# Optimization experiments

Hardware: AMD Instinct MI355X
Metric: run time of the kernel (lower is better)

## Reference

```python
import jax, jax.numpy as jnp
import numpy as np

TAU = 2.0        # LIFNode tau
ALPHA = 4.0      # spikingjelly default surrogate Sigmoid alpha
EPS = 1e-5       # BatchNorm eps
NUM_HEADS = 8

@jax.custom_vjp
def spike(u):
    # Heaviside with sigmoid surrogate gradient (spikingjelly default)
    return (u >= 0.0).astype(u.dtype)

def _spike_fwd(u):
    return spike(u), u

def _spike_bwd(u, g):
    s = jax.nn.sigmoid(ALPHA * u)
    return (g * ALPHA * s * (1.0 - s),)

spike.defvjp(_spike_fwd, _spike_bwd)

def lif(x, vth=1.0):
    # single-step LIF from rest (v=0, v_reset=0, decay_input=True): v = x / tau
    return spike(x / TAU - vth)

def conv1x1_bn(x, w, gamma, beta, mean, var):
    # 1x1 conv (no bias) + eval-mode BatchNorm, fused affine
    y = jnp.einsum('oc,bchw->bohw', w, x)
    inv = gamma / jnp.sqrt(var + EPS)
    return y * inv[None, :, None, None] + (beta - mean * inv)[None, :, None, None]


def setup_inputs() -> dict:
    B, C, H, W = 16, 768, 32, 32
    key = jax.random.key(0)
    ks = jax.random.split(key, 22)
    def bn(i):
        return (jax.random.uniform(ks[i], (C,)) + 0.5,
                0.1 * jax.random.normal(ks[i + 1], (C,)),
                0.1 * jax.random.normal(ks[i + 2], (C,)),
                jax.random.uniform(ks[i + 3], (C,)) + 0.5)
    q_gamma, q_beta, q_mean, q_var = bn(1)
    k_gamma, k_beta, k_mean, k_var = bn(5)
    v_gamma, v_beta, v_mean, v_var = bn(9)
    p_gamma, p_beta, p_mean, p_var = bn(13)
    W_SCALE = 0.25  # keeps post-BN activations spanning the LIF threshold
    return {
        'x': 3.0 * jax.random.normal(ks[0], (B, C, H, W), dtype=jnp.float32),
        'wq': W_SCALE * jax.random.normal(ks[17], (C, C), dtype=jnp.float32),
        'q_gamma': q_gamma, 'q_beta': q_beta, 'q_mean': q_mean, 'q_var': q_var,
        'wk': W_SCALE * jax.random.normal(ks[18], (C, C), dtype=jnp.float32),
        'k_gamma': k_gamma, 'k_beta': k_beta, 'k_mean': k_mean, 'k_var': k_var,
        'wv': W_SCALE * jax.random.normal(ks[19], (C, C), dtype=jnp.float32),
        'v_gamma': v_gamma, 'v_beta': v_beta, 'v_mean': v_mean, 'v_var': v_var,
        'wp': W_SCALE * jax.random.normal(ks[20], (C, C), dtype=jnp.float32),
        'bp': 0.1 * jax.random.normal(ks[21], (C,), dtype=jnp.float32),
        'p_gamma': p_gamma, 'p_beta': p_beta, 'p_mean': p_mean, 'p_var': p_var,
    }


def reference(x, wq, q_gamma, q_beta, q_mean, q_var,
              wk, k_gamma, k_beta, k_mean, k_var,
              wv, v_gamma, v_beta, v_mean, v_var,
              wp, bp, p_gamma, p_beta, p_mean, p_var):
    B, C, H, W = x.shape
    N = H * W
    h = NUM_HEADS
    hd = C // h
    identity = x
    xs = lif(x)  # shortcut_lif

    def branch(w, g, b, m, vv):
        y = lif(conv1x1_bn(xs, w, g, b, m, vv))            # [B,C,H,W] binary spikes
        y = y.reshape(B, C, N).transpose(0, 2, 1)           # [B,N,C]
        return y.reshape(B, N, h, hd).transpose(0, 2, 1, 3)  # [B,h,N,hd]

    q = branch(wq, q_gamma, q_beta, q_mean, q_var)
    k = branch(wk, k_gamma, k_beta, k_mean, k_var)
    v = branch(wv, v_gamma, v_beta, v_mean, v_var)

    kv = jnp.sum(k * v, axis=2, keepdims=True)  # [B,h,1,hd] token reduction
    kv = lif(kv, vth=0.5)                       # attn_lif

    out = q * kv                                          # [B,h,N,hd]
    out = out.transpose(0, 2, 1, 3).reshape(B, N, C)      # [B,N,C]
    out = out.transpose(0, 2, 1).reshape(B, C, H, W)      # [B,C,H,W]

    y = jnp.einsum('oc,bchw->bohw', wp, out) + bp[None, :, None, None]
    inv = p_gamma / jnp.sqrt(p_var + EPS)
    y = y * inv[None, :, None, None] + (p_beta - p_mean * inv)[None, :, None, None]
    return y + identity
```

## Files before the change

### kernel.cpp

```cpp
#include <hip/hip_runtime.h>
#include <cstdint>
#include <cstddef>

#define C_DIM 768
#define NPIX  1024
#define B_DIM 16
#define NTOT  16384
#define KT_N  12
#define MT_N  6
#define JT_N  128
#define MT2_N 12
#define TAU   2.0e-3f
#define BCAP  64
#define NBLK  (3 * MT2_N * JT_N)
#define PLANE_B (C_DIM * C_DIM)
#define TILE_B  8192
#define AKT_B   (MT_N * TILE_B)

typedef __attribute__((ext_vector_type(4)))  int   int4v;
typedef __attribute__((ext_vector_type(16))) char  char16v;

__device__ __forceinline__ void gload16(const void* g, void* l) {
    __builtin_amdgcn_global_load_lds(
        (const __attribute__((address_space(1))) unsigned int*)g,
        (__attribute__((address_space(3))) unsigned int*)l, 16, 0, 0);
}

__global__ __launch_bounds__(256) void prep_weights(
    const float* __restrict__ w0, const float* __restrict__ w1,
    const float* __restrict__ w2, const float* __restrict__ w3,
    char* __restrict__ wall)
{
    const int tile = blockIdx.x;
    const int set  = blockIdx.y;
    const int kt = tile / MT_N, mt = tile % MT_N;
    const float* w = set == 0 ? w0 : set == 1 ? w1 : set == 2 ? w2 : w3;
    char* pl = wall + (size_t)set * 2 * PLANE_B;
#pragma unroll
    for (int i = 0; i < 2; ++i) {
        int q = threadIdx.x + i * 256;
        int kg = q >> 7, m = q & 127;
        int o = mt * 128 + m;
        int cbase = kt * 64 + kg * 16;
        char16v H, L;
#pragma unroll
        for (int e = 0; e < 16; ++e) {
            float wv = w[(size_t)o * C_DIM + cbase + e];
            int w16 = (int)lrintf(wv * 16384.0f);
            w16 = w16 > 32639 ? 32639 : (w16 < -32639 ? -32639 : w16);
            int hi = (w16 + 128) >> 8;
            int lo = w16 - (hi << 8);
            H[e] = (char)hi;
            L[e] = (char)lo;
        }
        size_t base = (size_t)tile * TILE_B + (size_t)q * 16;
        *(char16v*)(pl + base)           = H;
        *(char16v*)(pl + PLANE_B + base) = L;
    }
}

__global__ __launch_bounds__(256) void prep_bn(
    const float* __restrict__ qg, const float* __restrict__ qb,
    const float* __restrict__ qm, const float* __restrict__ qv,
    const float* __restrict__ kg, const float* __restrict__ kb,
    const float* __restrict__ km, const float* __restrict__ kv,
    const float* __restrict__ vg, const float* __restrict__ vb,
    const float* __restrict__ vm, const float* __restrict__ vv,
    const float* __restrict__ pg, const float* __restrict__ pb,
    const float* __restrict__ pm, const float* __restrict__ pv,
    float* __restrict__ invt, float* __restrict__ biast)
{
    int i = blockIdx.x * 256 + threadIdx.x;
    if (i >= 4 * C_DIM) return;
    int set = i / C_DIM, o = i - set * C_DIM;
    const float* g = set == 0 ? qg : set == 1 ? kg : set == 2 ? vg : pg;
    const float* b = set == 0 ? qb : set == 1 ? kb : set == 2 ? vb : pb;
    const float* m = set == 0 ? qm : set == 1 ? km : set == 2 ? vm : pm;
    const float* v = set == 0 ? qv : set == 1 ? kv : set == 2 ? vv : pv;
    float inv = g[o] / sqrtf(v[o] + 1e-5f);
    invt[i]  = inv;
    biast[i] = b[o] - m[o] * inv;
}

__global__ __launch_bounds__(256) void prep_spikes(
    const float* __restrict__ x, char* __restrict__ xs)
{
    const int jt = blockIdx.x;
    const int kt = blockIdx.y;
    const int b  = jt >> 3;
    const int n0 = (jt & 7) * 128;
#pragma unroll
    for (int i = 0; i < 2; ++i) {
        int q = threadIdx.x + i * 256;
        int kg = q >> 7, col = q & 127;
        char16v sv;
#pragma unroll
        for (int e = 0; e < 16; ++e) {
            float xv = x[((size_t)b * C_DIM + (kt * 64 + kg * 16 + e)) * NPIX + n0 + col];
            sv[e] = (xv >= 2.0f) ? (char)1 : (char)0;
        }
        *(char16v*)(xs + (size_t)(jt * KT_N + kt) * TILE_B + (size_t)q * 16) = sv;
    }
}

__global__ __launch_bounds__(256, 4) void branch_mfma(
    const char* __restrict__ wall, const char* __restrict__ xsblob,
    const float* __restrict__ invt, const float* __restrict__ biast,
    char* __restrict__ sall,
    unsigned int* __restrict__ cntArr, unsigned int* __restrict__ recsB)
{
    __shared__ char bstage[2][8192];
    __shared__ unsigned int lcnt;
    const int jt = blockIdx.x, mt = blockIdx.y, z = blockIdx.z;
    const int tid = threadIdx.x;
    const int lane = tid & 63, wid = tid >> 6;
    const int wm = wid >> 1, wn = wid & 1;
    const int lr = lane & 15, kg = lane >> 4;
    const char* wblob = wall + (size_t)z * 2 * PLANE_B;
    char* sblob = sall + (size_t)z * C_DIM * NTOT;
    const float* invz  = invt  + z * C_DIM;
    const float* biasz = biast + z * C_DIM;
    const unsigned int blk = ((unsigned)z * MT2_N + mt) * JT_N + jt;

    int4v acch[2][4], accl[2][4];
#pragma unroll
    for (int a = 0; a < 2; ++a)
#pragma unroll
        for (int b2 = 0; b2 < 4; ++b2) {
            acch[a][b2] = (int4v){0, 0, 0, 0};
            accl[a][b2] = (int4v){0, 0, 0, 0};
        }

    const int rb0 = mt * 64 + wm * 32 + lr;
    const int rb1 = rb0 + 16;
    const size_t aoff0 = (size_t)(rb0 >> 7) * TILE_B + kg * 2048 + (rb0 & 127) * 16;
    const size_t aoff1 = (size_t)(rb1 >> 7) * TILE_B + kg * 2048 + (rb1 & 127) * 16;

#define STAGE_B(buf, ktA) do {                                                \
        const char* Bb_ = xsblob + (size_t)(jt * KT_N + (ktA)) * TILE_B;      \
        gload16(Bb_ + (size_t)tid * 16,        bstage[buf] + tid * 16);       \
        gload16(Bb_ + 4096 + (size_t)tid * 16, bstage[buf] + 4096 + tid * 16);\
    } while (0)

    int4v ah0c = *(const int4v*)(wblob + aoff0);
    int4v ah1c = *(const int4v*)(wblob + aoff1);
    int4v al0c = *(const int4v*)(wblob + PLANE_B + aoff0);
    int4v al1c = *(const int4v*)(wblob + PLANE_B + aoff1);
    STAGE_B(0, 0);
    if (tid == 0) lcnt = 0;
    __syncthreads();
    int cur = 0;
    for (int kt = 0; kt < KT_N; ++kt) {
        int4v ah0n, ah1n, al0n, al1n;
        bool more = (kt + 1 < KT_N);
        if (more) {
            STAGE_B(cur ^ 1, kt + 1);
            const char* wk = wblob + (size_t)(kt + 1) * AKT_B;
            ah0n = *(const int4v*)(wk + aoff0);
            ah1n = *(const int4v*)(wk + aoff1);
            al0n = *(const int4v*)(wk + PLANE_B + aoff0);
            al1n = *(const int4v*)(wk + PLANE_B + aoff1);
        }
        const char* st = bstage[cur];
        int4v bfr[4];
#pragma unroll
        for (int fn = 0; fn < 4; ++fn)
            bfr[fn] = *(const int4v*)&st[kg * 2048 + (wn * 64 + fn * 16 + lr) * 16];
#pragma unroll
        for (int fn = 0; fn < 4; ++fn) {
            acch[0][fn] = __builtin_amdgcn_mfma_i32_16x16x64_i8(ah0c, bfr[fn], acch[0][fn], 0, 0, 0);
            acch[1][fn] = __builtin_amdgcn_mfma_i32_16x16x64_i8(ah1c, bfr[fn], acch[1][fn], 0, 0, 0);
            accl[0][fn] = __builtin_amdgcn_mfma_i32_16x16x64_i8(al0c, bfr[fn], accl[0][fn], 0, 0, 0);
            accl[1][fn] = __builtin_amdgcn_mfma_i32_16x16x64_i8(al1c, bfr[fn], accl[1][fn], 0, 0, 0);
        }
        __syncthreads();
        if (more) { ah0c = ah0n; ah1c = ah1n; al0c = al0n; al1c = al1n; }
        cur ^= 1;
    }
#undef STAGE_B

    unsigned int pk[2][4];
#pragma unroll
    for (int fm = 0; fm < 2; ++fm)
#pragma unroll
        for (int fn = 0; fn < 4; ++fn) {
            unsigned int p = 0;
#pragma unroll
            for (int r = 0; r < 4; ++r) {
                int o = mt * 64 + wm * 32 + fm * 16 + kg * 4 + r;
                int vi = acch[fm][fn][r] * 256 + accl[fm][fn][r];
                float y = (float)vi * 6.103515625e-05f;
                float ybn = y * invz[o] + biasz[o];
                if (ybn >= 2.0f) p |= (1u << (r * 8));
                if (fabsf(ybn - 2.0f) < TAU) {
                    unsigned int idx = atomicAdd(&lcnt, 1u);
                    if (idx < BCAP) {
                        int j = jt * 128 + wn * 64 + fn * 16 + lr;
                        recsB[(size_t)blk * BCAP + idx] =
                            ((unsigned)z << 24) | ((unsigned)o << 14) | (unsigned)j;
                    }
                }
            }
            pk[fm][fn] = p;
        }

#pragma unroll
    for (int fnPair = 0; fnPair < 2; ++fnPair) {
        unsigned int got[4];
#pragma unroll
        for (int t = 0; t < 4; ++t) {
            int sel = (kg + t) & 3;
            int sfm = sel >> 1, sfn = (sel & 1) * 2 + fnPair;
            unsigned int send =
                sfm == 0 ? (sfn == 0 ? pk[0][0] : sfn == 1 ? pk[0][1] : sfn == 2 ? pk[0][2] : pk[0][3])
                         : (sfn == 0 ? pk[1][0] : sfn == 1 ? pk[1][1] : sfn == 2 ? pk[1][2] : pk[1][3]);
            int src = (((kg - t) & 3) << 4) + lr;
            got[t] = (unsigned int)__shfl((int)send, src);
        }
        unsigned int part[4];
#pragma unroll
        for (int j = 0; j < 4; ++j) {
            int tsel = (kg - j) & 3;
            part[j] = tsel == 0 ? got[0] : tsel == 1 ? got[1]
                    : tsel == 2 ? got[2] : got[3];
        }
        int4v chunk = (int4v){(int)part[0], (int)part[1], (int)part[2], (int)part[3]};
        int kg2 = wm * 2 + (kg >> 1);
        int col = wn * 64 + ((kg & 1) * 2 + fnPair) * 16 + lr;
        size_t off = (size_t)(jt * KT_N + mt) * TILE_B + (size_t)kg2 * 2048 + (size_t)col * 16;
        *(int4v*)(sblob + off) = chunk;
    }
    __syncthreads();
    if (tid == 0) {
        unsigned int c = lcnt;
        cntArr[blk] = c > BCAP ? BCAP : c;
    }
}

__global__ __launch_bounds__(256) void fixup(
    const char* __restrict__ xs,
    const float* __restrict__ wq, const float* __restrict__ wk, const float* __restrict__ wv,
    const float* __restrict__ qg, const float* __restrict__ qb, const float* __restrict__ qm, const float* __restrict__ qv,
    const float* __restrict__ kg, const float* __restrict__ kb2, const float* __restrict__ km, const float* __restrict__ kvr,
    const float* __restrict__ vg, const float* __restrict__ vb, const float* __restrict__ vm, const float* __restrict__ vv,
    char* __restrict__ sq, char* __restrict__ sk, char* __restrict__ sv,
    const unsigned int* __restrict__ cntArr, const unsigned int* __restrict__ recsB)
{
#pragma clang fp contract(off)
    __shared__ float cw[4][C_DIM];
    const int lane = threadIdx.x & 63;
    const int wvid = threadIdx.x >> 6;
    const int gwave = blockIdx.x * 4 + wvid;
    const int nwaves = gridDim.x * 4;
    const int npairs = NBLK * BCAP;

    for (int p = gwave; p < npairs; p += nwaves) {
        int slot = p / NBLK;
        int reg  = p - slot * NBLK;
        if ((unsigned)slot >= cntArr[reg]) continue;
        unsigned int rec = recsB[(size_t)reg * BCAP + slot];
        int plane = rec >> 24, o = (rec >> 14) & 1023, j = rec & 16383;
        int jt = j >> 7, col = j & 127;
        const float* w = plane == 0 ? wq : plane == 1 ? wk : wv;
        int base = 0;
#pragma unroll
        for (int cc = 0; cc < 12; ++cc) {
            int c = cc * 64 + lane;
            char s = xs[(size_t)(jt * KT_N + (c >> 6)) * TILE_B
                        + ((c >> 4) & 3) * 2048 + col * 16 + (c & 15)];
            float wvv = w[(size_t)o * C_DIM + c];
            bool act = (s != 0);
            unsigned long long m = __ballot(act);
            int pos = __popcll(m & ((1ull << lane) - 1ull));
            if (act) cw[wvid][base + pos] = wvv;
            base += __popcll(m);
        }
        __builtin_amdgcn_s_waitcnt(0);
        if (lane == 0) {
            float s = 0.0f;
            for (int i = 0; i < base; ++i) s = s + cw[wvid][i];
            const float* g  = plane == 0 ? qg : plane == 1 ? kg : vg;
            const float* be = plane == 0 ? qb : plane == 1 ? kb2 : vb;
            const float* me = plane == 0 ? qm : plane == 1 ? km : vm;
            const float* va = plane == 0 ? qv : plane == 1 ? kvr : vv;
            float invv = g[o] / sqrtf(va[o] + 1e-5f);
            float t1 = me[o] * invv;
            float bias = be[o] - t1;
            float t3 = s * invv;
            float ybn = t3 + bias;
            char spv = (ybn >= 2.0f) ? (char)1 : (char)0;
            char* blob = plane == 0 ? sq : plane == 1 ? sk : sv;
            blob[(size_t)(jt * KT_N + (o >> 6)) * TILE_B
                 + ((o >> 4) & 3) * 2048 + col * 16 + (o & 15)] = spv;
        }
    }
}

__global__ __launch_bounds__(256) void kv_mask_blob(
    const char* __restrict__ sk, const char* __restrict__ sv,
    unsigned char* __restrict__ maskb)
{
    const int kt = blockIdx.x, b = blockIdx.y;
    const int t = threadIdx.x;
    const int kg = t >> 6;
    const int col0 = (t & 63) * 2;
    __shared__ unsigned int lmask[4][4];
    if (t < 16) lmask[t >> 2][t & 3] = 0;
    __syncthreads();
    uint4 acc = make_uint4(0, 0, 0, 0);
    for (int jti = 0; jti < 8; ++jti) {
        size_t base = (size_t)((b * 8 + jti) * KT_N + kt) * TILE_B + kg * 2048;
#pragma unroll
        for (int cc = 0; cc < 2; ++cc) {
            uint4 kk = *(const uint4*)(sk + base + (size_t)(col0 + cc) * 16);
            uint4 vv = *(const uint4*)(sv + base + (size_t)(col0 + cc) * 16);
            acc.x |= (kk.x & vv.x); acc.y |= (kk.y & vv.y);
            acc.z |= (kk.z & vv.z); acc.w |= (kk.w & vv.w);
        }
    }
    if (acc.x) atomicOr(&lmask[kg][0], acc.x);
    if (acc.y) atomicOr(&lmask[kg][1], acc.y);
    if (acc.z) atomicOr(&lmask[kg][2], acc.z);
    if (acc.w) atomicOr(&lmask[kg][3], acc.w);
    __syncthreads();
    if (t < 64) {
        int kg2 = t >> 4, e = t & 15;
        unsigned int dw = lmask[kg2][e >> 2];
        unsigned char byte = (dw >> ((e & 3) * 8)) & 0xFF;
        maskb[(size_t)b * C_DIM + kt * 64 + t] = byte ? 1 : 0;
    }
}

__global__ __launch_bounds__(256, 4) void final_mfma(
    const char* __restrict__ wblob, const char* __restrict__ sqblob,
    const unsigned char* __restrict__ maskb,
    const float* __restrict__ x, const float* __restrict__ bp,
    const float* __restrict__ invt, const float* __restrict__ biast,
    float* __restrict__ out)
{
    __shared__ char bstage[2][8192];
    const int jt = blockIdx.x, mt = blockIdx.y;
    const int tid = threadIdx.x;
    const int lane = tid & 63, wid = tid >> 6;
    const int wm = wid >> 1, wn = wid & 1;
    const int lr = lane & 15, kg = lane >> 4;
    const int b = jt >> 3;
    const float* invp  = invt  + 3 * C_DIM;
    const float* biasp = biast + 3 * C_DIM;

    int4v acch[2][4], accl[2][4];
#pragma unroll
    for (int a = 0; a < 2; ++a)
#pragma unroll
        for (int b2 = 0; b2 < 4; ++b2) {
            acch[a][b2] = (int4v){0, 0, 0, 0};
            accl[a][b2] = (int4v){0, 0, 0, 0};
        }

    const int rb0 = mt * 64 + wm * 32 + lr;
    const int rb1 = rb0 + 16;
    const size_t aoff0 = (size_t)(rb0 >> 7) * TILE_B + kg * 2048 + (rb0 & 127) * 16;
    const size_t aoff1 = (size_t)(rb1 >> 7) * TILE_B + kg * 2048 + (rb1 & 127) * 16;
    const unsigned char* Mbase = maskb + (size_t)b * C_DIM + kg * 16;

#define STAGE_B(buf, ktA) do {                                                \
        const char* Bb_ = sqblob + (size_t)(jt * KT_N + (ktA)) * TILE_B;      \
        gload16(Bb_ + (size_t)tid * 16,        bstage[buf] + tid * 16);       \
        gload16(Bb_ + 4096 + (size_t)tid * 16, bstage[buf] + 4096 + tid * 16);\
    } while (0)

    int4v ah0c = *(const int4v*)(wblob + aoff0);
    int4v ah1c = *(const int4v*)(wblob + aoff1);
    int4v al0c = *(const int4v*)(wblob + PLANE_B + aoff0);
    int4v al1c = *(const int4v*)(wblob + PLANE_B + aoff1);
    STAGE_B(0, 0);
    __syncthreads();
    int cur = 0;
    for (int kt = 0; kt < KT_N; ++kt) {
        int4v ah0n, ah1n, al0n, al1n;
        bool more = (kt + 1 < KT_N);
        if (more) {
            STAGE_B(cur ^ 1, kt + 1);
            const char* wk = wblob + (size_t)(kt + 1) * AKT_B;
            ah0n = *(const int4v*)(wk + aoff0);
            ah1n = *(const int4v*)(wk + aoff1);
            al0n = *(const int4v*)(wk + PLANE_B + aoff0);
            al1n = *(const int4v*)(wk + PLANE_B + aoff1);
        }
        int4v mp = *(const int4v*)(Mbase + kt * 64);
        const char* st = bstage[cur];
        int4v bfr[4];
#pragma unroll
        for (int fn = 0; fn < 4; ++fn) {
            bfr[fn] = *(const int4v*)&st[kg * 2048 + (wn * 64 + fn * 16 + lr) * 16];
            bfr[fn] &= mp;
        }
#pragma unroll
        for (int fn = 0; fn < 4; ++fn) {
            acch[0][fn] = __builtin_amdgcn_mfma_i32_16x16x64_i8(ah0c, bfr[fn], acch[0][fn], 0, 0, 0);
            acch[1][fn] = __builtin_amdgcn_mfma_i32_16x16x64_i8(ah1c, bfr[fn], acch[1][fn], 0, 0, 0);
            accl[0][fn] = __builtin_amdgcn_mfma_i32_16x16x64_i8(al0c, bfr[fn], accl[0][fn], 0, 0, 0);
            accl[1][fn] = __builtin_amdgcn_mfma_i32_16x16x64_i8(al1c, bfr[fn], accl[1][fn], 0, 0, 0);
        }
        __syncthreads();
        if (more) { ah0c = ah0n; ah1c = ah1n; al0c = al0n; al1c = al1n; }
        cur ^= 1;
    }
#undef STAGE_B

    const int n0 = (jt & 7) * 128;
#pragma unroll
    for (int fm = 0; fm < 2; ++fm)
#pragma unroll
        for (int fn = 0; fn < 4; ++fn)
#pragma unroll
            for (int r = 0; r < 4; ++r) {
                int p = mt * 64 + wm * 32 + fm * 16 + kg * 4 + r;
                int nl = wn * 64 + fn * 16 + lr;
                int vi = acch[fm][fn][r] * 256 + accl[fm][fn][r];
                float pre = (float)vi * 6.103515625e-05f;
                size_t idx = ((size_t)b * C_DIM + p) * NPIX + n0 + nl;
                out[idx] = (pre + bp[p]) * invp[p] + biasp[p] + x[idx];
            }
}

extern "C" void kernel_launch(void* const* d_in, const int* in_sizes, int n_in,
                              void* d_out, int out_size, void* d_ws, size_t ws_size,
                              hipStream_t stream) {
    const float* x  = (const float*)d_in[0];
    const float* wq = (const float*)d_in[1];
    const float* qg = (const float*)d_in[2];
    const float* qb = (const float*)d_in[3];
    const float* qm = (const float*)d_in[4];
    const float* qv = (const float*)d_in[5];
    const float* wk = (const float*)d_in[6];
    const float* kg = (const float*)d_in[7];
    const float* kb = (const float*)d_in[8];
    const float* km = (const float*)d_in[9];
    const float* kvv= (const float*)d_in[10];
    const float* wv = (const float*)d_in[11];
    const float* vg = (const float*)d_in[12];
    const float* vb = (const float*)d_in[13];
    const float* vm = (const float*)d_in[14];
    const float* vv = (const float*)d_in[15];
    const float* wp = (const float*)d_in[16];
    const float* bp = (const float*)d_in[17];
    const float* pg = (const float*)d_in[18];
    const float* pb = (const float*)d_in[19];
    const float* pm = (const float*)d_in[20];
    const float* pv = (const float*)d_in[21];

    const size_t SPIKE = (size_t)C_DIM * NTOT;
    char* sq  = (char*)d_ws;
    char* sk  = sq + SPIKE;
    char* sv  = sk + SPIKE;
    char* xs  = sv + SPIKE;
    char* wall = xs + SPIKE;
    unsigned char* maskb = (unsigned char*)(wall + (size_t)4 * 2 * PLANE_B);
    unsigned int* cntArr = (unsigned int*)(maskb + 16384);
    unsigned int* recsB  = cntArr + NBLK;
    float* invt  = (float*)(recsB + (size_t)NBLK * BCAP);
    float* biast = invt + 4 * C_DIM;
    char* wpb = wall + (size_t)3 * 2 * PLANE_B;

    prep_weights<<<dim3(KT_N * MT_N, 4), 256, 0, stream>>>(wq, wk, wv, wp, wall);
    prep_bn<<<12, 256, 0, stream>>>(qg, qb, qm, qv, kg, kb, km, kvv,
                                    vg, vb, vm, vv, pg, pb, pm, pv, invt, biast);
    prep_spikes<<<dim3(JT_N, KT_N), 256, 0, stream>>>(x, xs);
    branch_mfma<<<dim3(JT_N, MT2_N, 3), 256, 0, stream>>>(
        wall, xs, invt, biast, sq, cntArr, recsB);
    fixup<<<2048, 256, 0, stream>>>(xs, wq, wk, wv,
                                    qg, qb, qm, qv, kg, kb, km, kvv, vg, vb, vm, vv,
                                    sq, sk, sv, cntArr, recsB);
    kv_mask_blob<<<dim3(KT_N, B_DIM), 256, 0, stream>>>(sk, sv, maskb);
    final_mfma<<<dim3(JT_N, MT2_N), 256, 0, stream>>>(
        wpb, sq, maskb, x, bp, invt, biast, (float*)d_out);
}
```

Measured before the change: 173.0 us.

## Stage full spike panel in LDS and loop over q/k/v in one block

Both MFMA kernels now load the whole 96KB activation panel for a column tile into shared memory once. Blocks grow to 512 threads covering 128 output rows, so the per-k-step double buffering and barriers go away. The branch kernel also iterates over the three q/k/v projections inside one block, reusing the staged panel instead of launching a z dimension. The cost is much larger LDS use per block and fewer blocks (768 instead of 4608/1536), which lowers occupancy and parallelism. The fixup record count array is now indexed per (mt,jt) and shared across z, which changes the BCAP budget per block.

```diff
diff --git a/kernel.cpp b/kernel.cpp
--- a/kernel.cpp
+++ b/kernel.cpp
@@ -9,13 +9,12 @@
 #define KT_N  12
 #define MT_N  6
 #define JT_N  128
-#define MT2_N 12
 #define TAU   2.0e-3f
 #define BCAP  64
-#define NBLK  (3 * MT2_N * JT_N)
+#define NBLK  (MT_N * JT_N)
 #define PLANE_B (C_DIM * C_DIM)
 #define TILE_B  8192
-#define AKT_B   (MT_N * TILE_B)
+#define SPIKE_B ((size_t)C_DIM * NTOT)
 
 typedef __attribute__((ext_vector_type(4)))  int   int4v;
 typedef __attribute__((ext_vector_type(16))) char  char16v;
@@ -103,132 +102,128 @@
     }
 }
 
-__global__ __launch_bounds__(256, 4) void branch_mfma(
+__global__ __launch_bounds__(512, 2) void branch_mfma(
     const char* __restrict__ wall, const char* __restrict__ xsblob,
     const float* __restrict__ invt, const float* __restrict__ biast,
     char* __restrict__ sall,
     unsigned int* __restrict__ cntArr, unsigned int* __restrict__ recsB)
 {
-    __shared__ char bstage[2][8192];
+    __shared__ char panel[KT_N * TILE_B];
     __shared__ unsigned int lcnt;
-    const int jt = blockIdx.x, mt = blockIdx.y, z = blockIdx.z;
+    const int jt = blockIdx.x, mt = blockIdx.y;
     const int tid = threadIdx.x;
     const int lane = tid & 63, wid = tid >> 6;
     const int wm = wid >> 1, wn = wid & 1;
     const int lr = lane & 15, kg = lane >> 4;
-    const char* wblob = wall + (size_t)z * 2 * PLANE_B;
-    char* sblob = sall + (size_t)z * C_DIM * NTOT;
-    const float* invz  = invt  + z * C_DIM;
-    const float* biasz = biast + z * C_DIM;
-    const unsigned int blk = ((unsigned)z * MT2_N + mt) * JT_N + jt;
-
-    int4v acch[2][4], accl[2][4];
-#pragma unroll
-    for (int a = 0; a < 2; ++a)
-#pragma unroll
-        for (int b2 = 0; b2 < 4; ++b2) {
-            acch[a][b2] = (int4v){0, 0, 0, 0};
-            accl[a][b2] = (int4v){0, 0, 0, 0};
-        }
-
-    const int rb0 = mt * 64 + wm * 32 + lr;
-    const int rb1 = rb0 + 16;
-    const size_t aoff0 = (size_t)(rb0 >> 7) * TILE_B + kg * 2048 + (rb0 & 127) * 16;
-    const size_t aoff1 = (size_t)(rb1 >> 7) * TILE_B + kg * 2048 + (rb1 & 127) * 16;
-
-#define STAGE_B(buf, ktA) do {                                                \
-        const char* Bb_ = xsblob + (size_t)(jt * KT_N + (ktA)) * TILE_B;      \
-        gload16(Bb_ + (size_t)tid * 16,        bstage[buf] + tid * 16);       \
-        gload16(Bb_ + 4096 + (size_t)tid * 16, bstage[buf] + 4096 + tid * 16);\
-    } while (0)
-
-    int4v ah0c = *(const int4v*)(wblob + aoff0);
-    int4v ah1c = *(const int4v*)(wblob + aoff1);
-    int4v al0c = *(const int4v*)(wblob + PLANE_B + aoff0);
-    int4v al1c = *(const int4v*)(wblob + PLANE_B + aoff1);
-    STAGE_B(0, 0);
+    const unsigned int blk = (unsigned)mt * JT_N + jt;
+
+    const char* Bp = xsblob + (size_t)jt * KT_N * TILE_B;
+#pragma unroll
+    for (int i = 0; i < 12; ++i)
+        gload16(Bp + (size_t)(tid + i * 512) * 16, panel + (tid + i * 512) * 16);
     if (tid == 0) lcnt = 0;
     __syncthreads();
-    int cur = 0;
-    for (int kt = 0; kt < KT_N; ++kt) {
-        int4v ah0n, ah1n, al0n, al1n;
-        bool more = (kt + 1 < KT_N);
-        if (more) {
-            STAGE_B(cur ^ 1, kt + 1);
-            const char* wk = wblob + (size_t)(kt + 1) * AKT_B;
-            ah0n = *(const int4v*)(wk + aoff0);
-            ah1n = *(const int4v*)(wk + aoff1);
-            al0n = *(const int4v*)(wk + PLANE_B + aoff0);
-            al1n = *(const int4v*)(wk + PLANE_B + aoff1);
-        }
-        const char* st = bstage[cur];
-        int4v bfr[4];
-#pragma unroll
-        for (int fn = 0; fn < 4; ++fn)
-            bfr[fn] = *(const int4v*)&st[kg * 2048 + (wn * 64 + fn * 16 + lr) * 16];
-#pragma unroll
-        for (int fn = 0; fn < 4; ++fn) {
-            acch[0][fn] = __builtin_amdgcn_mfma_i32_16x16x64_i8(ah0c, bfr[fn], acch[0][fn], 0, 0, 0);
-            acch[1][fn] = __builtin_amdgcn_mfma_i32_16x16x64_i8(ah1c, bfr[fn], acch[1][fn], 0, 0, 0);
-            accl[0][fn] = __builtin_amdgcn_mfma_i32_16x16x64_i8(al0c, bfr[fn], accl[0][fn], 0, 0, 0);
-            accl[1][fn] = __builtin_amdgcn_mfma_i32_16x16x64_i8(al1c, bfr[fn], accl[1][fn], 0, 0, 0);
-        }
-        __syncthreads();
-        if (more) { ah0c = ah0n; ah1c = ah1n; al0c = al0n; al1c = al1n; }
-        cur ^= 1;
-    }
-#undef STAGE_B
-
-    unsigned int pk[2][4];
-#pragma unroll
-    for (int fm = 0; fm < 2; ++fm)
-#pragma unroll
-        for (int fn = 0; fn < 4; ++fn) {
-            unsigned int p = 0;
-#pragma unroll
-            for (int r = 0; r < 4; ++r) {
-                int o = mt * 64 + wm * 32 + fm * 16 + kg * 4 + r;
-                int vi = acch[fm][fn][r] * 256 + accl[fm][fn][r];
-                float y = (float)vi * 6.103515625e-05f;
-                float ybn = y * invz[o] + biasz[o];
-                if (ybn >= 2.0f) p |= (1u << (r * 8));
-                if (fabsf(ybn - 2.0f) < TAU) {
-                    unsigned int idx = atomicAdd(&lcnt, 1u);
-                    if (idx < BCAP) {
-                        int j = jt * 128 + wn * 64 + fn * 16 + lr;
-                        recsB[(size_t)blk * BCAP + idx] =
-                            ((unsigned)z << 24) | ((unsigned)o << 14) | (unsigned)j;
+
+    const int aoffs = kg * 2048 + (wm * 32 + lr) * 16;
+
+    for (int z = 0; z < 3; ++z) {
+        const char* wblob = wall + (size_t)z * 2 * PLANE_B;
+        char* sblob = sall + (size_t)z * SPIKE_B;
+        const float* invz  = invt  + z * C_DIM;
+        const float* biasz = biast + z * C_DIM;
+
+        int4v acch[2][4], accl[2][4];
+#pragma unroll
+        for (int a = 0; a < 2; ++a)
+#pragma unroll
+            for (int b2 = 0; b2 < 4; ++b2) {
+                acch[a][b2] = (int4v){0, 0, 0, 0};
+                accl[a][b2] = (int4v){0, 0, 0, 0};
+            }
+
+        const char* A0 = wblob + (size_t)mt * TILE_B;
+        int4v ah0c = *(const int4v*)(A0 + aoffs);
+        int4v ah1c = *(const int4v*)(A0 + aoffs + 256);
+        int4v al0c = *(const int4v*)(A0 + PLANE_B + aoffs);
+        int4v al1c = *(const int4v*)(A0 + PLANE_B + aoffs + 256);
+
+        for (int kt = 0; kt < KT_N; ++kt) {
+            int4v ah0n, ah1n, al0n, al1n;
+            bool more = (kt + 1 < KT_N);
+            if (more) {
+                const char* An = wblob + (size_t)((kt + 1) * MT_N + mt) * TILE_B;
+                ah0n = *(const int4v*)(An + aoffs);
+                ah1n = *(const int4v*)(An + aoffs + 256);
+                al0n = *(const int4v*)(An + PLANE_B + aoffs);
+                al1n = *(const int4v*)(An + PLANE_B + aoffs + 256);
+            }
+            const char* st = panel + kt * TILE_B;
+            int4v bfr[4];
+#pragma unroll
+            for (int fn = 0; fn < 4; ++fn)
+                bfr[fn] = *(const int4v*)&st[kg * 2048 + (wn * 64 + fn * 16 + lr) * 16];
+#pragma unroll
+            for (int fn = 0; fn < 4; ++fn) {
+                acch[0][fn] = __builtin_amdgcn_mfma_i32_16x16x64_i8(ah0c, bfr[fn], acch[0][fn], 0, 0, 0);
+                acch[1][fn] = __builtin_amdgcn_mfma_i32_16x16x64_i8(ah1c, bfr[fn], acch[1][fn], 0, 0, 0);
+                accl[0][fn] = __builtin_amdgcn_mfma_i32_16x16x64_i8(al0c, bfr[fn], accl[0][fn], 0, 0, 0);
+                accl[1][fn] = __builtin_amdgcn_mfma_i32_16x16x64_i8(al1c, bfr[fn], accl[1][fn], 0, 0, 0);
+            }
+            if (more) { ah0c = ah0n; ah1c = ah1n; al0c = al0n; al1c = al1n; }
+        }
+
+        unsigned int pk[2][4];
+#pragma unroll
+        for (int fm = 0; fm < 2; ++fm)
+#pragma unroll
+            for (int fn = 0; fn < 4; ++fn) {
+                unsigned int p = 0;
+#pragma unroll
+                for (int r = 0; r < 4; ++r) {
+                    int o = mt * 128 + wm * 32 + fm * 16 + kg * 4 + r;
+                    int vi = acch[fm][fn][r] * 256 + accl[fm][fn][r];
+                    float y = (float)vi * 6.103515625e-05f;
+                    float ybn = y * invz[o] + biasz[o];
+                    if (ybn >= 2.0f) p |= (1u << (r * 8));
+                    if (fabsf(ybn - 2.0f) < TAU) {
+                        unsigned int idx = atomicAdd(&lcnt, 1u);
+                        if (idx < BCAP) {
+                            int j = jt * 128 + wn * 64 + fn * 16 + lr;
+                            recsB[(size_t)blk * BCAP + idx] =
+                                ((unsigned)z << 24) | ((unsigned)o << 14) | (unsigned)j;
+                        }
                     }
                 }
-            }
-            pk[fm][fn] = p;
-        }
-
-#pragma unroll
-    for (int fnPair = 0; fnPair < 2; ++fnPair) {
-        unsigned int got[4];
-#pragma unroll
-        for (int t = 0; t < 4; ++t) {
-            int sel = (kg + t) & 3;
-            int sfm = sel >> 1, sfn = (sel & 1) * 2 + fnPair;
-            unsigned int send =
-                sfm == 0 ? (sfn == 0 ? pk[0][0] : sfn == 1 ? pk[0][1] : sfn == 2 ? pk[0][2] : pk[0][3])
-                         : (sfn == 0 ? pk[1][0] : sfn == 1 ? pk[1][1] : sfn == 2 ? pk[1][2] : pk[1][3]);
-            int src = (((kg - t) & 3) << 4) + lr;
-            got[t] = (unsigned int)__shfl((int)send, src);
-        }
-        unsigned int part[4];
-#pragma unroll
-        for (int j = 0; j < 4; ++j) {
-            int tsel = (kg - j) & 3;
-            part[j] = tsel == 0 ? got[0] : tsel == 1 ? got[1]
-                    : tsel == 2 ? got[2] : got[3];
-        }
-        int4v chunk = (int4v){(int)part[0], (int)part[1], (int)part[2], (int)part[3]};
-        int kg2 = wm * 2 + (kg >> 1);
-        int col = wn * 64 + ((kg & 1) * 2 + fnPair) * 16 + lr;
-        size_t off = (size_t)(jt * KT_N + mt) * TILE_B + (size_t)kg2 * 2048 + (size_t)col * 16;
-        *(int4v*)(sblob + off) = chunk;
+                pk[fm][fn] = p;
+            }
+
+#pragma unroll
+        for (int fnPair = 0; fnPair < 2; ++fnPair) {
+            unsigned int got[4];
+#pragma unroll
+            for (int t = 0; t < 4; ++t) {
+                int sel = (kg + t) & 3;
+                int sfm = sel >> 1, sfn = (sel & 1) * 2 + fnPair;
+                unsigned int send =
+                    sfm == 0 ? (sfn == 0 ? pk[0][0] : sfn == 1 ? pk[0][1] : sfn == 2 ? pk[0][2] : pk[0][3])
+                             : (sfn == 0 ? pk[1][0] : sfn == 1 ? pk[1][1] : sfn == 2 ? pk[1][2] : pk[1][3]);
+                int src = (((kg - t) & 3) << 4) + lr;
+                got[t] = (unsigned int)__shfl((int)send, src);
+            }
+            unsigned int part[4];
+#pragma unroll
+            for (int j = 0; j < 4; ++j) {
+                int tsel = (kg - j) & 3;
+                part[j] = tsel == 0 ? got[0] : tsel == 1 ? got[1]
+                        : tsel == 2 ? got[2] : got[3];
+            }
+            int4v chunk = (int4v){(int)part[0], (int)part[1], (int)part[2], (int)part[3]};
+            int kt2 = mt * 2 + (wm >> 1);
+            int kg2 = (wm & 1) * 2 + (kg >> 1);
+            int col = wn * 64 + ((kg & 1) * 2 + fnPair) * 16 + lr;
+            size_t off = (size_t)(jt * KT_N + kt2) * TILE_B + (size_t)kg2 * 2048 + (size_t)col * 16;
+            *(int4v*)(sblob + off) = chunk;
+        }
     }
     __syncthreads();
     if (tid == 0) {
@@ -331,14 +326,14 @@
     }
 }
 
-__global__ __launch_bounds__(256, 4) void final_mfma(
+__global__ __launch_bounds__(512, 2) void final_mfma(
     const char* __restrict__ wblob, const char* __restrict__ sqblob,
     const unsigned char* __restrict__ maskb,
     const float* __restrict__ x, const float* __restrict__ bp,
     const float* __restrict__ invt, const float* __restrict__ biast,
     float* __restrict__ out)
 {
-    __shared__ char bstage[2][8192];
+    __shared__ char panel[KT_N * TILE_B];
     const int jt = blockIdx.x, mt = blockIdx.y;
     const int tid = threadIdx.x;
     const int lane = tid & 63, wid = tid >> 6;
@@ -348,6 +343,15 @@
     const float* invp  = invt  + 3 * C_DIM;
     const float* biasp = biast + 3 * C_DIM;
 
+    const char* Bp = sqblob + (size_t)jt * KT_N * TILE_B;
+#pragma unroll
+    for (int i = 0; i < 12; ++i)
+        gload16(Bp + (size_t)(tid + i * 512) * 16, panel + (tid + i * 512) * 16);
+    __syncthreads();
+
+    const int aoffs = kg * 2048 + (wm * 32 + lr) * 16;
+    const unsigned char* Mbase = maskb + (size_t)b * C_DIM + kg * 16;
+
     int4v acch[2][4], accl[2][4];
 #pragma unroll
     for (int a = 0; a < 2; ++a)
@@ -357,38 +361,24 @@
             accl[a][b2] = (int4v){0, 0, 0, 0};
         }
 
-    const int rb0 = mt * 64 + wm * 32 + lr;
-    const int rb1 = rb0 + 16;
-    const size_t aoff0 = (size_t)(rb0 >> 7) * TILE_B + kg * 2048 + (rb0 & 127) * 16;
-    const size_t aoff1 = (size_t)(rb1 >> 7) * TILE_B + kg * 2048 + (rb1 & 127) * 16;
-    const unsigned char* Mbase = maskb + (size_t)b * C_DIM + kg * 16;
-
-#define STAGE_B(buf, ktA) do {                                                \
-        const char* Bb_ = sqblob + (size_t)(jt * KT_N + (ktA)) * TILE_B;      \
-        gload16(Bb_ + (size_t)tid * 16,        bstage[buf] + tid * 16);       \
-        gload16(Bb_ + 4096 + (size_t)tid * 16, bstage[buf] + 4096 + tid * 16);\
-    } while (0)
-
-    int4v ah0c = *(const int4v*)(wblob + aoff0);
-    int4v ah1c = *(const int4v*)(wblob + aoff1);
-    int4v al0c = *(const int4v*)(wblob + PLANE_B + aoff0);
-    int4v al1c = *(const int4v*)(wblob + PLANE_B + aoff1);
-    STAGE_B(0, 0);
-    __syncthreads();
-    int cur = 0;
+    const char* A0 = wblob + (size_t)mt * TILE_B;
+    int4v ah0c = *(const int4v*)(A0 + aoffs);
+    int4v ah1c = *(const int4v*)(A0 + aoffs + 256);
+    int4v al0c = *(const int4v*)(A0 + PLANE_B + aoffs);
+    int4v al1c = *(const int4v*)(A0 + PLANE_B + aoffs + 256);
+
     for (int kt = 0; kt < KT_N; ++kt) {
         int4v ah0n, ah1n, al0n, al1n;
         bool more = (kt + 1 < KT_N);
         if (more) {
-            STAGE_B(cur ^ 1, kt + 1);
-            const char* wk = wblob + (size_t)(kt + 1) * AKT_B;
-            ah0n = *(const int4v*)(wk + aoff0);
-            ah1n = *(const int4v*)(wk + aoff1);
-            al0n = *(const int4v*)(wk + PLANE_B + aoff0);
-            al1n = *(const int4v*)(wk + PLANE_B + aoff1);
+            const char* An = wblob + (size_t)((kt + 1) * MT_N + mt) * TILE_B;
+            ah0n = *(const int4v*)(An + aoffs);
+            ah1n = *(const int4v*)(An + aoffs + 256);
+            al0n = *(const int4v*)(An + PLANE_B + aoffs);
+            al1n = *(const int4v*)(An + PLANE_B + aoffs + 256);
         }
         int4v mp = *(const int4v*)(Mbase + kt * 64);
-        const char* st = bstage[cur];
+        const char* st = panel + kt * TILE_B;
         int4v bfr[4];
 #pragma unroll
         for (int fn = 0; fn < 4; ++fn) {
@@ -402,11 +392,8 @@
             accl[0][fn] = __builtin_amdgcn_mfma_i32_16x16x64_i8(al0c, bfr[fn], accl[0][fn], 0, 0, 0);
             accl[1][fn] = __builtin_amdgcn_mfma_i32_16x16x64_i8(al1c, bfr[fn], accl[1][fn], 0, 0, 0);
         }
-        __syncthreads();
         if (more) { ah0c = ah0n; ah1c = ah1n; al0c = al0n; al1c = al1n; }
-        cur ^= 1;
-    }
-#undef STAGE_B
+    }
 
     const int n0 = (jt & 7) * 128;
 #pragma unroll
@@ -415,7 +402,7 @@
         for (int fn = 0; fn < 4; ++fn)
 #pragma unroll
             for (int r = 0; r < 4; ++r) {
-                int p = mt * 64 + wm * 32 + fm * 16 + kg * 4 + r;
+                int p = mt * 128 + wm * 32 + fm * 16 + kg * 4 + r;
                 int nl = wn * 64 + fn * 16 + lr;
                 int vi = acch[fm][fn][r] * 256 + accl[fm][fn][r];
                 float pre = (float)vi * 6.103515625e-05f;
@@ -450,12 +437,11 @@
     const float* pm = (const float*)d_in[20];
     const float* pv = (const float*)d_in[21];
 
-    const size_t SPIKE = (size_t)C_DIM * NTOT;
     char* sq  = (char*)d_ws;
-    char* sk  = sq + SPIKE;
-    char* sv  = sk + SPIKE;
-    char* xs  = sv + SPIKE;
-    char* wall = xs + SPIKE;
+    char* sk  = sq + SPIKE_B;
+    char* sv  = sk + SPIKE_B;
+    char* xs  = sv + SPIKE_B;
+    char* wall = xs + SPIKE_B;
     unsigned char* maskb = (unsigned char*)(wall + (size_t)4 * 2 * PLANE_B);
     unsigned int* cntArr = (unsigned int*)(maskb + 16384);
     unsigned int* recsB  = cntArr + NBLK;
@@ -467,12 +453,12 @@
     prep_bn<<<12, 256, 0, stream>>>(qg, qb, qm, qv, kg, kb, km, kvv,
                                     vg, vb, vm, vv, pg, pb, pm, pv, invt, biast);
     prep_spikes<<<dim3(JT_N, KT_N), 256, 0, stream>>>(x, xs);
-    branch_mfma<<<dim3(JT_N, MT2_N, 3), 256, 0, stream>>>(
+    branch_mfma<<<dim3(JT_N, MT_N), 512, 0, stream>>>(
         wall, xs, invt, biast, sq, cntArr, recsB);
     fixup<<<2048, 256, 0, stream>>>(xs, wq, wk, wv,
                                     qg, qb, qm, qv, kg, kb, km, kvv, vg, vb, vm, vv,
                                     sq, sk, sv, cntArr, recsB);
     kv_mask_blob<<<dim3(KT_N, B_DIM), 256, 0, stream>>>(sk, sv, maskb);
-    final_mfma<<<dim3(JT_N, MT2_N), 256, 0, stream>>>(
+    final_mfma<<<dim3(JT_N, MT_N), 512, 0, stream>>>(
         wpb, sq, maskb, x, bp, invt, biast, (float*)d_out);
 }
```

Measured after the change: 286.3 us. 1.65x slower.

## Stage weight tiles through LDS with two-ahead async prefetch in MFMA kernels

Applied to the files above, without the earlier changes.

Both int8 MFMA GEMM kernels now stage the A (weight hi/lo planes) tiles into LDS alongside B via global_load_lds, instead of loading A fragments directly from global memory into registers. The loop prefetches two k-tiles ahead, using explicit vmcnt/lgkmcnt waits, raw s_barrier and sched_barrier, and s_setprio around the MFMA block. The final kernel also caches the per-batch mask in LDS. This aims to hide global latency and cut register pressure, at the cost of doubled LDS per block, which may lower occupancy, and fragile hand-written wait counts.

```diff
diff --git a/kernel.cpp b/kernel.cpp
--- a/kernel.cpp
+++ b/kernel.cpp
@@ -15,7 +15,6 @@
 #define NBLK  (3 * MT2_N * JT_N)
 #define PLANE_B (C_DIM * C_DIM)
 #define TILE_B  8192
-#define AKT_B   (MT_N * TILE_B)
 
 typedef __attribute__((ext_vector_type(4)))  int   int4v;
 typedef __attribute__((ext_vector_type(16))) char  char16v;
@@ -109,7 +108,7 @@
     char* __restrict__ sall,
     unsigned int* __restrict__ cntArr, unsigned int* __restrict__ recsB)
 {
-    __shared__ char bstage[2][8192];
+    __shared__ char stage[2][16384];
     __shared__ unsigned int lcnt;
     const int jt = blockIdx.x, mt = blockIdx.y, z = blockIdx.z;
     const int tid = threadIdx.x;
@@ -117,11 +116,26 @@
     const int wm = wid >> 1, wn = wid & 1;
     const int lr = lane & 15, kg = lane >> 4;
     const char* wblob = wall + (size_t)z * 2 * PLANE_B;
-    char* sblob = sall + (size_t)z * C_DIM * NTOT;
+    char* sblob = sall + (size_t)z * (size_t)C_DIM * NTOT;
     const float* invz  = invt  + z * C_DIM;
     const float* biasz = biast + z * C_DIM;
     const unsigned int blk = ((unsigned)z * MT2_N + mt) * JT_N + jt;
 
+    const int s_kg = tid >> 6, s_m = tid & 63;
+    const int mt128 = mt >> 1, mrow = (mt & 1) * 64;
+
+#define STG(buf, ktA) do {                                                     \
+        const char* Ab_ = wblob + (size_t)((ktA) * MT_N + mt128) * TILE_B;     \
+        const char* Bb_ = xsblob + (size_t)(jt * KT_N + (ktA)) * TILE_B;       \
+        char* d_ = stage[buf];                                                 \
+        gload16(Ab_ + s_kg * 2048 + (size_t)(mrow + s_m) * 16,                 \
+                d_ + s_kg * 1024 + s_m * 16);                                  \
+        gload16(Ab_ + PLANE_B + s_kg * 2048 + (size_t)(mrow + s_m) * 16,       \
+                d_ + 4096 + s_kg * 1024 + s_m * 16);                           \
+        gload16(Bb_ + (size_t)tid * 16,        d_ + 8192 + tid * 16);          \
+        gload16(Bb_ + 4096 + (size_t)tid * 16, d_ + 12288 + tid * 16);         \
+    } while (0)
+
     int4v acch[2][4], accl[2][4];
 #pragma unroll
     for (int a = 0; a < 2; ++a)
@@ -131,53 +145,42 @@
             accl[a][b2] = (int4v){0, 0, 0, 0};
         }
 
-    const int rb0 = mt * 64 + wm * 32 + lr;
-    const int rb1 = rb0 + 16;
-    const size_t aoff0 = (size_t)(rb0 >> 7) * TILE_B + kg * 2048 + (rb0 & 127) * 16;
-    const size_t aoff1 = (size_t)(rb1 >> 7) * TILE_B + kg * 2048 + (rb1 & 127) * 16;
-
-#define STAGE_B(buf, ktA) do {                                                \
-        const char* Bb_ = xsblob + (size_t)(jt * KT_N + (ktA)) * TILE_B;      \
-        gload16(Bb_ + (size_t)tid * 16,        bstage[buf] + tid * 16);       \
-        gload16(Bb_ + 4096 + (size_t)tid * 16, bstage[buf] + 4096 + tid * 16);\
-    } while (0)
-
-    int4v ah0c = *(const int4v*)(wblob + aoff0);
-    int4v ah1c = *(const int4v*)(wblob + aoff1);
-    int4v al0c = *(const int4v*)(wblob + PLANE_B + aoff0);
-    int4v al1c = *(const int4v*)(wblob + PLANE_B + aoff1);
-    STAGE_B(0, 0);
+    STG(0, 0);
+    STG(1, 1);
     if (tid == 0) lcnt = 0;
-    __syncthreads();
     int cur = 0;
+    const int arow = (wm * 32 + lr) * 16;
     for (int kt = 0; kt < KT_N; ++kt) {
-        int4v ah0n, ah1n, al0n, al1n;
-        bool more = (kt + 1 < KT_N);
-        if (more) {
-            STAGE_B(cur ^ 1, kt + 1);
-            const char* wk = wblob + (size_t)(kt + 1) * AKT_B;
-            ah0n = *(const int4v*)(wk + aoff0);
-            ah1n = *(const int4v*)(wk + aoff1);
-            al0n = *(const int4v*)(wk + PLANE_B + aoff0);
-            al1n = *(const int4v*)(wk + PLANE_B + aoff1);
-        }
-        const char* st = bstage[cur];
+        if (kt + 1 < KT_N) asm volatile("s_waitcnt vmcnt(4)");
+        else               asm volatile("s_waitcnt vmcnt(0)");
+        __builtin_amdgcn_s_barrier();
+        __builtin_amdgcn_sched_barrier(0);
+        const char* st = stage[cur];
+        int4v ah0 = *(const int4v*)&st[kg * 1024 + arow];
+        int4v ah1 = *(const int4v*)&st[kg * 1024 + arow + 256];
+        int4v al0 = *(const int4v*)&st[4096 + kg * 1024 + arow];
+        int4v al1 = *(const int4v*)&st[4096 + kg * 1024 + arow + 256];
         int4v bfr[4];
 #pragma unroll
         for (int fn = 0; fn < 4; ++fn)
-            bfr[fn] = *(const int4v*)&st[kg * 2048 + (wn * 64 + fn * 16 + lr) * 16];
+            bfr[fn] = *(const int4v*)&st[8192 + kg * 2048 + (wn * 64 + fn * 16 + lr) * 16];
+        __builtin_amdgcn_sched_barrier(0);
+        asm volatile("s_waitcnt lgkmcnt(0)");
+        __builtin_amdgcn_sched_barrier(0);
+        __builtin_amdgcn_s_barrier();
+        if (kt + 2 < KT_N) STG(cur, kt + 2);
+        __builtin_amdgcn_s_setprio(1);
 #pragma unroll
         for (int fn = 0; fn < 4; ++fn) {
-            acch[0][fn] = __builtin_amdgcn_mfma_i32_16x16x64_i8(ah0c, bfr[fn], acch[0][fn], 0, 0, 0);
-            acch[1][fn] = __builtin_amdgcn_mfma_i32_16x16x64_i8(ah1c, bfr[fn], acch[1][fn], 0, 0, 0);
-            accl[0][fn] = __builtin_amdgcn_mfma_i32_16x16x64_i8(al0c, bfr[fn], accl[0][fn], 0, 0, 0);
-            accl[1][fn] = __builtin_amdgcn_mfma_i32_16x16x64_i8(al1c, bfr[fn], accl[1][fn], 0, 0, 0);
-        }
-        __syncthreads();
-        if (more) { ah0c = ah0n; ah1c = ah1n; al0c = al0n; al1c = al1n; }
+            acch[0][fn] = __builtin_amdgcn_mfma_i32_16x16x64_i8(ah0, bfr[fn], acch[0][fn], 0, 0, 0);
+            acch[1][fn] = __builtin_amdgcn_mfma_i32_16x16x64_i8(ah1, bfr[fn], acch[1][fn], 0, 0, 0);
+            accl[0][fn] = __builtin_amdgcn_mfma_i32_16x16x64_i8(al0, bfr[fn], accl[0][fn], 0, 0, 0);
+            accl[1][fn] = __builtin_amdgcn_mfma_i32_16x16x64_i8(al1, bfr[fn], accl[1][fn], 0, 0, 0);
+        }
+        __builtin_amdgcn_s_setprio(0);
         cur ^= 1;
     }
-#undef STAGE_B
+#undef STG
 
     unsigned int pk[2][4];
 #pragma unroll
@@ -338,7 +341,8 @@
     const float* __restrict__ invt, const float* __restrict__ biast,
     float* __restrict__ out)
 {
-    __shared__ char bstage[2][8192];
+    __shared__ char stage[2][16384];
+    __shared__ char mlds[768];
     const int jt = blockIdx.x, mt = blockIdx.y;
     const int tid = threadIdx.x;
     const int lane = tid & 63, wid = tid >> 6;
@@ -348,6 +352,21 @@
     const float* invp  = invt  + 3 * C_DIM;
     const float* biasp = biast + 3 * C_DIM;
 
+    const int s_kg = tid >> 6, s_m = tid & 63;
+    const int mt128 = mt >> 1, mrow = (mt & 1) * 64;
+
+#define STG(buf, ktA) do {                                                     \
+        const char* Ab_ = wblob + (size_t)((ktA) * MT_N + mt128) * TILE_B;     \
+        const char* Bb_ = sqblob + (size_t)(jt * KT_N + (ktA)) * TILE_B;       \
+        char* d_ = stage[buf];                                                 \
+        gload16(Ab_ + s_kg * 2048 + (size_t)(mrow + s_m) * 16,                 \
+                d_ + s_kg * 1024 + s_m * 16);                                  \
+        gload16(Ab_ + PLANE_B + s_kg * 2048 + (size_t)(mrow + s_m) * 16,       \
+                d_ + 4096 + s_kg * 1024 + s_m * 16);                           \
+        gload16(Bb_ + (size_t)tid * 16,        d_ + 8192 + tid * 16);          \
+        gload16(Bb_ + 4096 + (size_t)tid * 16, d_ + 12288 + tid * 16);         \
+    } while (0)
+
     int4v acch[2][4], accl[2][4];
 #pragma unroll
     for (int a = 0; a < 2; ++a)
@@ -357,56 +376,47 @@
             accl[a][b2] = (int4v){0, 0, 0, 0};
         }
 
-    const int rb0 = mt * 64 + wm * 32 + lr;
-    const int rb1 = rb0 + 16;
-    const size_t aoff0 = (size_t)(rb0 >> 7) * TILE_B + kg * 2048 + (rb0 & 127) * 16;
-    const size_t aoff1 = (size_t)(rb1 >> 7) * TILE_B + kg * 2048 + (rb1 & 127) * 16;
-    const unsigned char* Mbase = maskb + (size_t)b * C_DIM + kg * 16;
-
-#define STAGE_B(buf, ktA) do {                                                \
-        const char* Bb_ = sqblob + (size_t)(jt * KT_N + (ktA)) * TILE_B;      \
-        gload16(Bb_ + (size_t)tid * 16,        bstage[buf] + tid * 16);       \
-        gload16(Bb_ + 4096 + (size_t)tid * 16, bstage[buf] + 4096 + tid * 16);\
-    } while (0)
-
-    int4v ah0c = *(const int4v*)(wblob + aoff0);
-    int4v ah1c = *(const int4v*)(wblob + aoff1);
-    int4v al0c = *(const int4v*)(wblob + PLANE_B + aoff0);
-    int4v al1c = *(const int4v*)(wblob + PLANE_B + aoff1);
-    STAGE_B(0, 0);
+    if (tid < 48)
+        *(int4v*)&mlds[tid * 16] = *(const int4v*)(maskb + (size_t)b * C_DIM + tid * 16);
+    STG(0, 0);
+    STG(1, 1);
     __syncthreads();
     int cur = 0;
+    const int arow = (wm * 32 + lr) * 16;
     for (int kt = 0; kt < KT_N; ++kt) {
-        int4v ah0n, ah1n, al0n, al1n;
-        bool more = (kt + 1 < KT_N);
-        if (more) {
-            STAGE_B(cur ^ 1, kt + 1);
-            const char* wk = wblob + (size_t)(kt + 1) * AKT_B;
-            ah0n = *(const int4v*)(wk + aoff0);
-            ah1n = *(const int4v*)(wk + aoff1);
-            al0n = *(const int4v*)(wk + PLANE_B + aoff0);
-            al1n = *(const int4v*)(wk + PLANE_B + aoff1);
-        }
-        int4v mp = *(const int4v*)(Mbase + kt * 64);
-        const char* st = bstage[cur];
+        if (kt + 1 < KT_N) asm volatile("s_waitcnt vmcnt(4)");
+        else               asm volatile("s_waitcnt vmcnt(0)");
+        __builtin_amdgcn_s_barrier();
+        __builtin_amdgcn_sched_barrier(0);
+        const char* st = stage[cur];
+        int4v ah0 = *(const int4v*)&st[kg * 1024 + arow];
+        int4v ah1 = *(const int4v*)&st[kg * 1024 + arow + 256];
+        int4v al0 = *(const int4v*)&st[4096 + kg * 1024 + arow];
+        int4v al1 = *(const int4v*)&st[4096 + kg * 1024 + arow + 256];
+        int4v mp = *(const int4v*)&mlds[kt * 64 + kg * 16];
         int4v bfr[4];
 #pragma unroll
+        for (int fn = 0; fn < 4; ++fn)
+            bfr[fn] = *(const int4v*)&st[8192 + kg * 2048 + (wn * 64 + fn * 16 + lr) * 16];
+        __builtin_amdgcn_sched_barrier(0);
+        asm volatile("s_waitcnt lgkmcnt(0)");
+        __builtin_amdgcn_sched_barrier(0);
+        __builtin_amdgcn_s_barrier();
+        if (kt + 2 < KT_N) STG(cur, kt + 2);
+#pragma unroll
+        for (int fn = 0; fn < 4; ++fn) bfr[fn] &= mp;
+        __builtin_amdgcn_s_setprio(1);
+#pragma unroll
         for (int fn = 0; fn < 4; ++fn) {
-            bfr[fn] = *(const int4v*)&st[kg * 2048 + (wn * 64 + fn * 16 + lr) * 16];
-            bfr[fn] &= mp;
-        }
-#pragma unroll
-        for (int fn = 0; fn < 4; ++fn) {
-            acch[0][fn] = __builtin_amdgcn_mfma_i32_16x16x64_i8(ah0c, bfr[fn], acch[0][fn], 0, 0, 0);
-            acch[1][fn] = __builtin_amdgcn_mfma_i32_16x16x64_i8(ah1c, bfr[fn], acch[1][fn], 0, 0, 0);
-            accl[0][fn] = __builtin_amdgcn_mfma_i32_16x16x64_i8(al0c, bfr[fn], accl[0][fn], 0, 0, 0);
-            accl[1][fn] = __builtin_amdgcn_mfma_i32_16x16x64_i8(al1c, bfr[fn], accl[1][fn], 0, 0, 0);
-        }
-        __syncthreads();
-        if (more) { ah0c = ah0n; ah1c = ah1n; al0c = al0n; al1c = al1n; }
+            acch[0][fn] = __builtin_amdgcn_mfma_i32_16x16x64_i8(ah0, bfr[fn], acch[0][fn], 0, 0, 0);
+            acch[1][fn] = __builtin_amdgcn_mfma_i32_16x16x64_i8(ah1, bfr[fn], acch[1][fn], 0, 0, 0);
+            accl[0][fn] = __builtin_amdgcn_mfma_i32_16x16x64_i8(al0, bfr[fn], accl[0][fn], 0, 0, 0);
+            accl[1][fn] = __builtin_amdgcn_mfma_i32_16x16x64_i8(al1, bfr[fn], accl[1][fn], 0, 0, 0);
+        }
+        __builtin_amdgcn_s_setprio(0);
         cur ^= 1;
     }
-#undef STAGE_B
+#undef STG
 
     const int n0 = (jt & 7) * 128;
 #pragma unroll
```

Measured after the change: 159.8 us. 1.08x faster.
